# Kernel optimization log

Measured on AMD Instinct MI355X. Metric: run time of the kernel, lower is better.

The kernel has to match this reference:

```python
import jax, jax.numpy as jnp
import numpy as np

B, S, H, E = 8, 2048, 1024, 8

def setup_inputs() -> dict:
    key = jax.random.key(0)
    ks = jax.random.split(key, 7)
    sc = 1.0 / np.sqrt(H)
    return {
        "x":   jax.random.normal(ks[0], (B, S, H), dtype=jnp.float32),
        "We":  jax.random.normal(ks[1], (E, H, H), dtype=jnp.float32) * sc,
        "be":  jax.random.normal(ks[2], (E, H), dtype=jnp.float32) * 0.01,
        "Wr1": jax.random.normal(ks[3], (H, H), dtype=jnp.float32) * sc,
        "br1": jax.random.normal(ks[4], (H,), dtype=jnp.float32) * 0.01,
        "Wr2": jax.random.normal(ks[5], (H, E), dtype=jnp.float32) * sc,
        "br2": jax.random.normal(ks[6], (E,), dtype=jnp.float32) * 0.01,
    }

def reference(x, We, be, Wr1, br1, Wr2, br2):
    # Router: mean over seq -> Linear+ReLU -> Linear -> softmax over experts
    x_mean = x.mean(axis=1)                                   # [B,H]
    h = jax.nn.relu(x_mean @ Wr1 + br1)                        # [B,H]
    routing = jax.nn.softmax(h @ Wr2 + br2, axis=-1)           # [B,E]
    # Dense all-experts MLP: every expert processes every token
    eo = jax.nn.relu(jnp.einsum('bsh,ehd->ebsd', x, We)
                     + be[:, None, None, :])                   # [E,B,S,H]
    # KV caches are zero-initialized and read before any update in the
    # original forward, so their additive contribution is zero here.
    out = jnp.einsum('ebsd,be->bsd', eo, routing)              # [B,S,H]
    return out
```

## Files before the change

kernel.cpp:

```cpp
#include <hip/hip_runtime.h>
#include <stdint.h>

#define Hdim 1024
#define Bdim 8
#define Sdim 2048
#define Edim 8
#define Mtot 16384
#define Ntot 8192

typedef short bf16x8 __attribute__((ext_vector_type(8)));
typedef unsigned short u16x8 __attribute__((ext_vector_type(8)));
typedef float f32x4 __attribute__((ext_vector_type(4)));

__device__ __forceinline__ unsigned short f2bf(float f) {
  union { float f; unsigned u; } v; v.f = f;
  unsigned r = (v.u + 0x7FFFu + ((v.u >> 16) & 1u)) >> 16;
  return (unsigned short)r;
}

__device__ __forceinline__ void gload16(const void* g, void* l) {
  __builtin_amdgcn_global_load_lds((const __attribute__((address_space(1))) void*)g,
                                   (__attribute__((address_space(3))) void*)l,
                                   16, 0, 0);
}

#define VMCNT_(N) asm volatile("s_waitcnt vmcnt(" #N ")" ::: "memory")
#define VMCNT(N) VMCNT_(N)
#define BAR() __builtin_amdgcn_s_barrier()

__global__ void k_convert_mean(const float* __restrict__ x,
                               unsigned short* __restrict__ xb,
                               float* __restrict__ part) {
  const int b = blockIdx.y;
  const int s0 = blockIdx.x * 32;
  const int t = threadIdx.x;
  const int hg = (t & 127) << 3;
  const int sp = t >> 7;
  float accv[8];
#pragma unroll
  for (int q = 0; q < 8; ++q) accv[q] = 0.f;
#pragma unroll 4
  for (int i = 0; i < 16; ++i) {
    const int s = s0 + sp + (i << 1);
    const size_t base = ((size_t)b * Sdim + s) * Hdim + hg;
    const float4 lo = *(const float4*)(x + base);
    const float4 hi = *(const float4*)(x + base + 4);
    accv[0] += lo.x; accv[1] += lo.y; accv[2] += lo.z; accv[3] += lo.w;
    accv[4] += hi.x; accv[5] += hi.y; accv[6] += hi.z; accv[7] += hi.w;
    u16x8 pk;
    pk[0] = f2bf(lo.x); pk[1] = f2bf(lo.y); pk[2] = f2bf(lo.z); pk[3] = f2bf(lo.w);
    pk[4] = f2bf(hi.x); pk[5] = f2bf(hi.y); pk[6] = f2bf(hi.z); pk[7] = f2bf(hi.w);
    *(u16x8*)(xb + base) = pk;
  }
  float* pp = part + ((size_t)b * 128 + blockIdx.x * 2 + sp) * Hdim + hg;
#pragma unroll
  for (int q = 0; q < 8; ++q) pp[q] = accv[q];
}

__global__ void k_transpose_w(const float* __restrict__ We,
                              unsigned short* __restrict__ wt) {
  __shared__ float lds[64][65];
  const int e = blockIdx.z, hb = blockIdx.y, db = blockIdx.x;
  const int t = threadIdx.x;
  const float* src = We + ((size_t)e * Hdim + hb * 64) * Hdim + db * 64;
#pragma unroll 4
  for (int it = 0; it < 16; ++it) {
    int idx = it * 256 + t;
    int r = idx >> 6, c = idx & 63;
    lds[r][c] = src[(size_t)r * Hdim + c];
  }
  __syncthreads();
#pragma unroll 4
  for (int it = 0; it < 16; ++it) {
    int idx = it * 256 + t;
    int r = idx >> 6, c = idx & 63;
    const int np = (db * 64 + r) * 8 + e;
    wt[(size_t)np * Hdim + hb * 64 + c] = f2bf(lds[c][r]);
  }
}

__global__ void k_router1(const float* __restrict__ part,
                          const float* __restrict__ Wr1,
                          const float* __restrict__ br1,
                          float* __restrict__ hbuf) {
  __shared__ float xm[Hdim];
  const int b = blockIdx.y, jc = blockIdx.x, t = threadIdx.x;
  for (int k = t; k < Hdim; k += 256) {
    float s = 0.f;
    const float* p = part + (size_t)b * 128 * Hdim + k;
#pragma unroll 8
    for (int c = 0; c < 128; ++c) s += p[(size_t)c * Hdim];
    xm[k] = s * (1.0f / 2048.0f);
  }
  __syncthreads();
  const int j = jc * 256 + t;
  float acc = br1[j];
#pragma unroll 8
  for (int k = 0; k < Hdim; ++k) acc = fmaf(xm[k], Wr1[(size_t)k * Hdim + j], acc);
  hbuf[b * Hdim + j] = fmaxf(acc, 0.f);
}

__global__ void k_router2(const float* __restrict__ hbuf,
                          const float* __restrict__ Wr2,
                          const float* __restrict__ br2,
                          float* __restrict__ routing) {
  const int t = threadIdx.x;
  const int e = t & 7;
  const int b = t >> 3;
  float acc = br2[e];
  const float* hb = hbuf + b * Hdim;
#pragma unroll 8
  for (int k = 0; k < Hdim; ++k) acc = fmaf(hb[k], Wr2[k * Edim + e], acc);
  float m = acc;
  for (int d = 1; d < 8; d <<= 1) m = fmaxf(m, __shfl_xor(m, d, 64));
  float p = __expf(acc - m);
  float s = p;
  for (int d = 1; d < 8; d <<= 1) s += __shfl_xor(s, d, 64);
  routing[t] = p / s;
}

__global__ __launch_bounds__(512, 2)
void k_moe_gemm(const unsigned short* __restrict__ xb,
                const unsigned short* __restrict__ wt,
                const float* __restrict__ be,
                const float* __restrict__ routing,
                float* __restrict__ out) {
  extern __shared__ char smem[];
  const int t = threadIdx.x;
  const int wave = t >> 6, lane = t & 63;
  const int la15 = lane & 15;
  const int wr = wave >> 2;
  const int wcn = wave & 3;

  const int bid = blockIdx.x;
  const int wg = (bid & 7) * 256 + (bid >> 3);
  const int m0 = (wg >> 5) * 256;
  const int n0 = (wg & 31) * 256;

  const int cx = (((lane & 7) ^ (lane >> 3)) << 3);
  const unsigned short* aStage = xb + (size_t)(m0 + wave * 8 + (lane >> 3)) * Hdim + cx;
  const int bRowLoc = ((wave & 3) << 3) + ((wave >> 2) << 6) + (lane >> 3);
  const unsigned short* bStage = wt + (size_t)(n0 + bRowLoc) * Hdim + cx;
  const int aLdsW = wave * 1024;
  const int bLdsW = ((wave & 3) << 10) + ((wave >> 2) << 13);

  const int swz0 = (((lane >> 4) ^ (lane & 7)) << 4);
  const int swz1 = ((((lane >> 4) + 4) ^ (lane & 7)) << 4);
  const int aRd = (wr * 128 + la15) * 128;
  const int bRd = (wcn * 64 + la15) * 128;

  f32x4 acc[8][4];
#pragma unroll
  for (int i = 0; i < 8; ++i)
#pragma unroll
    for (int j = 0; j < 4; ++j) acc[i][j] = (f32x4){0.f, 0.f, 0.f, 0.f};

#define STG_A(half, buf, k0) do { \
    gload16(aStage + (half) * 64 * 1024 + (k0),          smem + (buf) * 32768 + aLdsW + (half) * 8192); \
    gload16(aStage + (128 + (half) * 64) * 1024 + (k0),  smem + (buf) * 32768 + aLdsW + 16384 + (half) * 8192); \
  } while (0)
#define STG_B(sub, buf, k0) do { \
    gload16(bStage + (sub) * 32 * 1024 + (k0),           smem + 65536 + (buf) * 32768 + bLdsW + (sub) * 4096); \
    gload16(bStage + (128 + (sub) * 32) * 1024 + (k0),   smem + 65536 + (buf) * 32768 + bLdsW + 16384 + (sub) * 4096); \
  } while (0)
#define LD_A(dst, buf, qi) do { \
    _Pragma("unroll") for (int ii = 0; ii < 4; ++ii) { \
      dst[ii][0] = *(const bf16x8*)(smem + (buf) * 32768 + aRd + (qi) * 8192 + ii * 2048 + swz0); \
      dst[ii][1] = *(const bf16x8*)(smem + (buf) * 32768 + aRd + (qi) * 8192 + ii * 2048 + swz1); } \
  } while (0)
#define LD_B(dst, buf, qj) do { \
    _Pragma("unroll") for (int jj = 0; jj < 2; ++jj) { \
      dst[jj][0] = *(const bf16x8*)(smem + 65536 + (buf) * 32768 + bRd + (qj) * 4096 + jj * 2048 + swz0); \
      dst[jj][1] = *(const bf16x8*)(smem + 65536 + (buf) * 32768 + bRd + (qj) * 4096 + jj * 2048 + swz1); } \
  } while (0)
#define MF_Q(af_, bf_, qi, jh) do { \
    __builtin_amdgcn_s_setprio(1); \
    _Pragma("unroll") for (int ii = 0; ii < 4; ++ii) \
      _Pragma("unroll") for (int jj = 0; jj < 2; ++jj) { \
        acc[(qi)*4+ii][(jh)*2+jj] = __builtin_amdgcn_mfma_f32_16x16x32_bf16(af_[ii][0], bf_[jj][0], acc[(qi)*4+ii][(jh)*2+jj], 0, 0, 0); \
        acc[(qi)*4+ii][(jh)*2+jj] = __builtin_amdgcn_mfma_f32_16x16x32_bf16(af_[ii][1], bf_[jj][1], acc[(qi)*4+ii][(jh)*2+jj], 0, 0, 0); } \
    __builtin_amdgcn_s_setprio(0); \
  } while (0)

  STG_A(0, 0, 0);
  STG_B(0, 0, 0);
  STG_B(1, 0, 0);
  STG_A(1, 0, 0);
  STG_A(0, 1, 64);
  STG_B(0, 1, 64);
  STG_B(1, 1, 64);
  VMCNT(8);
  BAR();

#pragma unroll 1
  for (int j = 0; j < 8; ++j) {
    const int kt1 = j * 128 + 64;
    const int kc2 = (j * 128 + 128) & 1023;
    const int kc3 = (j * 128 + 192) & 1023;
    bf16x8 afA[4][2], afB[4][2], bf0[2][2], bf1[2][2];
    VMCNT(8); LD_A(afA, 0, 0); LD_B(bf0, 0, 0); STG_A(1, 1, kt1);
    BAR(); MF_Q(afA, bf0, 0, 0); BAR();
    VMCNT(8); LD_B(bf1, 0, 1); STG_A(0, 0, kc2);
    BAR(); MF_Q(afA, bf1, 0, 1); BAR();
    VMCNT(8); LD_A(afB, 0, 1); STG_B(0, 0, kc2);
    BAR(); MF_Q(afB, bf1, 1, 1); BAR();
    VMCNT(8); STG_B(1, 0, kc2);
    BAR(); MF_Q(afB, bf0, 1, 0); BAR();
    VMCNT(8); LD_A(afA, 1, 0); LD_B(bf0, 1, 0); STG_A(1, 0, kc2);
    BAR(); MF_Q(afA, bf0, 0, 0); BAR();
    VMCNT(8); LD_B(bf1, 1, 1); STG_A(0, 1, kc3);
    BAR(); MF_Q(afA, bf1, 0, 1); BAR();
    VMCNT(8); LD_A(afB, 1, 1); STG_B(0, 1, kc3);
    BAR(); MF_Q(afB, bf1, 1, 1); BAR();
    VMCNT(8); STG_B(1, 1, kc3);
    BAR(); MF_Q(afB, bf0, 1, 0); BAR();
  }

  VMCNT(0);
  BAR();

  float* outb = (float*)smem;
  const int bidx = m0 >> 11;
  const float rw = routing[bidx * Edim + (lane & 7)];
  const int dblk = (lane >> 3) & 1;
  const bool writer = ((lane & 7) == 0);
#pragma unroll
  for (int j = 0; j < 4; ++j) {
    const int col0 = wcn * 64 + j * 16;
    const float bias = be[(lane & 7) * Hdim + (n0 >> 3) + (col0 >> 3) + dblk];
#pragma unroll
    for (int i = 0; i < 8; ++i) {
#pragma unroll
      for (int r = 0; r < 4; ++r) {
        float v = fmaxf(acc[i][j][r] + bias, 0.f) * rw;
        v += __shfl_xor(v, 1, 64);
        v += __shfl_xor(v, 2, 64);
        v += __shfl_xor(v, 4, 64);
        if (writer) {
          const int row = wr * 128 + i * 16 + ((lane >> 4) << 2) + r;
          outb[row * 33 + (col0 >> 3) + dblk] = v;
        }
      }
    }
  }
  BAR();
  const size_t obase = (size_t)m0 * Hdim + (n0 >> 3);
#pragma unroll
  for (int it = 0; it < 4; ++it) {
    const int r = it * 64 + (t >> 3);
    const int c = (t & 7) * 4;
    float4 vv;
    vv.x = outb[r * 33 + c];
    vv.y = outb[r * 33 + c + 1];
    vv.z = outb[r * 33 + c + 2];
    vv.w = outb[r * 33 + c + 3];
    *(float4*)(out + obase + (size_t)r * Hdim + c) = vv;
  }
#undef STG_A
#undef STG_B
#undef LD_A
#undef LD_B
#undef MF_Q
}

extern "C" void kernel_launch(void* const* d_in, const int* in_sizes, int n_in,
                              void* d_out, int out_size, void* d_ws, size_t ws_size,
                              hipStream_t stream) {
  const float* x   = (const float*)d_in[0];
  const float* We  = (const float*)d_in[1];
  const float* be  = (const float*)d_in[2];
  const float* Wr1 = (const float*)d_in[3];
  const float* br1 = (const float*)d_in[4];
  const float* Wr2 = (const float*)d_in[5];
  const float* br2 = (const float*)d_in[6];
  float* out = (float*)d_out;

  char* ws = (char*)d_ws;
  unsigned short* xb = (unsigned short*)ws;
  unsigned short* wt = (unsigned short*)(ws + 33554432);
  float* part    = (float*)(ws + 50331648);
  float* hbuf    = (float*)(ws + 54525952);
  float* routing = (float*)(ws + 54558720);

  hipFuncSetAttribute((const void*)k_moe_gemm,
                      hipFuncAttributeMaxDynamicSharedMemorySize, 131072);

  k_convert_mean<<<dim3(Sdim / 32, Bdim), 256, 0, stream>>>(x, xb, part);
  k_transpose_w<<<dim3(Hdim / 64, Hdim / 64, Edim), 256, 0, stream>>>(We, wt);
  k_router1<<<dim3(Hdim / 256, Bdim), 256, 0, stream>>>(part, Wr1, br1, hbuf);
  k_router2<<<1, 64, 0, stream>>>(hbuf, Wr2, br2, routing);
  k_moe_gemm<<<dim3(2048), 512, 131072, stream>>>(xb, wt, be, routing, out);
}
```

Measured before the change: 462.2 us.

## Software-pipeline LDS fragment loads ahead of MFMA phases with explicit lgkm waits

Restructures the GEMM main loop so that LDS-to-register fragment loads for the next MFMA phase are issued before the current phase's MFMAs. It splits A-fragment loads into halves and adds explicit lgkmcnt waits plus sched_barriers to pin the instruction order. Global-to-LDS staging is reordered, and the vmcnt waits are retuned to the new issue pattern. The aim is to hide LDS read latency behind matrix work, at the cost of more live fragment registers and fragile hand-tuned wait counts.

```diff
diff --git a/kernel.cpp b/kernel.cpp
--- a/kernel.cpp
+++ b/kernel.cpp
@@ -26,6 +26,9 @@
 
 #define VMCNT_(N) asm volatile("s_waitcnt vmcnt(" #N ")" ::: "memory")
 #define VMCNT(N) VMCNT_(N)
+#define LGKM_(N) asm volatile("s_waitcnt lgkmcnt(" #N ")" ::: "memory")
+#define LGKM(N) LGKM_(N)
+#define SCHED0() __builtin_amdgcn_sched_barrier(0)
 #define BAR() __builtin_amdgcn_s_barrier()
 
 __global__ void k_convert_mean(const float* __restrict__ x,
@@ -155,6 +158,8 @@
 #pragma unroll
     for (int j = 0; j < 4; ++j) acc[i][j] = (f32x4){0.f, 0.f, 0.f, 0.f};
 
+  bf16x8 a0[4][2], a1[4][2], b0[2][2], b1[2][2];
+
 #define STG_A(half, buf, k0) do { \
     gload16(aStage + (half) * 64 * 1024 + (k0),          smem + (buf) * 32768 + aLdsW + (half) * 8192); \
     gload16(aStage + (128 + (half) * 64) * 1024 + (k0),  smem + (buf) * 32768 + aLdsW + 16384 + (half) * 8192); \
@@ -165,6 +170,16 @@
   } while (0)
 #define LD_A(dst, buf, qi) do { \
     _Pragma("unroll") for (int ii = 0; ii < 4; ++ii) { \
+      dst[ii][0] = *(const bf16x8*)(smem + (buf) * 32768 + aRd + (qi) * 8192 + ii * 2048 + swz0); \
+      dst[ii][1] = *(const bf16x8*)(smem + (buf) * 32768 + aRd + (qi) * 8192 + ii * 2048 + swz1); } \
+  } while (0)
+#define LD_A_LO(dst, buf, qi) do { \
+    _Pragma("unroll") for (int ii = 0; ii < 2; ++ii) { \
+      dst[ii][0] = *(const bf16x8*)(smem + (buf) * 32768 + aRd + (qi) * 8192 + ii * 2048 + swz0); \
+      dst[ii][1] = *(const bf16x8*)(smem + (buf) * 32768 + aRd + (qi) * 8192 + ii * 2048 + swz1); } \
+  } while (0)
+#define LD_A_HI(dst, buf, qi) do { \
+    _Pragma("unroll") for (int ii = 2; ii < 4; ++ii) { \
       dst[ii][0] = *(const bf16x8*)(smem + (buf) * 32768 + aRd + (qi) * 8192 + ii * 2048 + swz0); \
       dst[ii][1] = *(const bf16x8*)(smem + (buf) * 32768 + aRd + (qi) * 8192 + ii * 2048 + swz1); } \
   } while (0)
@@ -183,37 +198,70 @@
   } while (0)
 
   STG_A(0, 0, 0);
+  STG_B(1, 0, 0);
   STG_B(0, 0, 0);
-  STG_B(1, 0, 0);
   STG_A(1, 0, 0);
   STG_A(0, 1, 64);
+  SCHED0();
+  STG_B(1, 1, 64);
   STG_B(0, 1, 64);
-  STG_B(1, 1, 64);
-  VMCNT(8);
+  STG_A(1, 1, 64);
+  VMCNT(6);
   BAR();
+  LD_A(a0, 0, 0);
+  SCHED0();
+  LD_B(b1, 0, 1);
 
 #pragma unroll 1
   for (int j = 0; j < 8; ++j) {
-    const int kt1 = j * 128 + 64;
-    const int kc2 = (j * 128 + 128) & 1023;
-    const int kc3 = (j * 128 + 192) & 1023;
-    bf16x8 afA[4][2], afB[4][2], bf0[2][2], bf1[2][2];
-    VMCNT(8); LD_A(afA, 0, 0); LD_B(bf0, 0, 0); STG_A(1, 1, kt1);
-    BAR(); MF_Q(afA, bf0, 0, 0); BAR();
-    VMCNT(8); LD_B(bf1, 0, 1); STG_A(0, 0, kc2);
-    BAR(); MF_Q(afA, bf1, 0, 1); BAR();
-    VMCNT(8); LD_A(afB, 0, 1); STG_B(0, 0, kc2);
-    BAR(); MF_Q(afB, bf1, 1, 1); BAR();
-    VMCNT(8); STG_B(1, 0, kc2);
-    BAR(); MF_Q(afB, bf0, 1, 0); BAR();
-    VMCNT(8); LD_A(afA, 1, 0); LD_B(bf0, 1, 0); STG_A(1, 0, kc2);
-    BAR(); MF_Q(afA, bf0, 0, 0); BAR();
-    VMCNT(8); LD_B(bf1, 1, 1); STG_A(0, 1, kc3);
-    BAR(); MF_Q(afA, bf1, 0, 1); BAR();
-    VMCNT(8); LD_A(afB, 1, 1); STG_B(0, 1, kc3);
-    BAR(); MF_Q(afB, bf1, 1, 1); BAR();
-    VMCNT(8); STG_B(1, 1, kc3);
-    BAR(); MF_Q(afB, bf0, 1, 0); BAR();
+    const int k2 = (j * 128 + 128) & 1023;
+    const int k3 = (j * 128 + 192) & 1023;
+    LD_B(b0, 0, 0);
+    SCHED0();
+    LD_A_LO(a1, 0, 1);
+    STG_A(0, 0, k2);
+    BAR(); LGKM(4); SCHED0();
+    MF_Q(a0, b0, 0, 0);
+    BAR();
+    LD_A_HI(a1, 0, 1);
+    STG_B(0, 0, k2);
+    BAR(); SCHED0();
+    MF_Q(a0, b1, 0, 1);
+    BAR();
+    LD_A(a0, 1, 0);
+    STG_B(1, 0, k2);
+    VMCNT(4);
+    BAR(); LGKM(8); SCHED0();
+    MF_Q(a1, b1, 1, 1);
+    BAR();
+    LD_B(b1, 1, 1);
+    STG_A(1, 0, k2);
+    BAR(); SCHED0();
+    MF_Q(a1, b0, 1, 0);
+    BAR();
+    LD_B(b0, 1, 0);
+    SCHED0();
+    LD_A_LO(a1, 1, 1);
+    STG_A(0, 1, k3);
+    BAR(); LGKM(4); SCHED0();
+    MF_Q(a0, b0, 0, 0);
+    BAR();
+    LD_A_HI(a1, 1, 1);
+    STG_B(0, 1, k3);
+    BAR(); SCHED0();
+    MF_Q(a0, b1, 0, 1);
+    BAR();
+    LD_A(a0, 0, 0);
+    STG_B(1, 1, k3);
+    VMCNT(4);
+    BAR(); LGKM(8); SCHED0();
+    MF_Q(a1, b1, 1, 1);
+    BAR();
+    LD_B(b1, 0, 1);
+    STG_A(1, 1, k3);
+    BAR(); SCHED0();
+    MF_Q(a1, b0, 1, 0);
+    BAR();
   }
 
   VMCNT(0);
@@ -259,6 +307,8 @@
 #undef STG_A
 #undef STG_B
 #undef LD_A
+#undef LD_A_LO
+#undef LD_A_HI
 #undef LD_B
 #undef MF_Q
 }
```

Result: no change. 464.0 us (+0.4%).
